# Performance work log

Measured on AMD Instinct MI355X. Metric: run time of the kernel, lower is better.

The kernel has to match this reference:

```python
import jax, jax.numpy as jnp
import numpy as np
import math

N = 5000; K = 30; E = N * K
C_S, C_Z, C_A = 256, 128, 16
H, DH, P, L = 4, 64, 8, 4
NUM_AA = 21
NUM_RBF = 16; D_MIN, D_MAX = 2.0, 22.0
EPS = 1e-8

def _ln(x):
    mu = jnp.mean(x, -1, keepdims=True)
    var = jnp.mean((x - mu) ** 2, -1, keepdims=True)
    return (x - mu) * jax.lax.rsqrt(var + 1e-5)

def _inv_apply(rot, trans, x):
    # rigid invert_apply: R^T (x - t); rot [n,3,3], trans [n,3], x [n,p,3]
    return jnp.einsum('nji,npj->npi', rot, x - trans[:, None, :])

def _rbf(d):
    mu = jnp.linspace(D_MIN, D_MAX, NUM_RBF)
    sigma = (D_MAX - D_MIN) / NUM_RBF
    return jnp.exp(-(((d[..., None] - mu) / sigma) ** 2))

def _dihedral_feats(bb):
    X = bb.reshape(-1, 3)  # [3N,3] N,CA,C chain
    dX = X[1:] - X[:-1]
    U = dX / (jnp.linalg.norm(dX, axis=-1, keepdims=True) + EPS)
    u2, u1, u0 = U[:-2], U[1:-1], U[2:]
    n2 = jnp.cross(u2, u1); n2 = n2 / (jnp.linalg.norm(n2, axis=-1, keepdims=True) + EPS)
    n1 = jnp.cross(u1, u0); n1 = n1 / (jnp.linalg.norm(n1, axis=-1, keepdims=True) + EPS)
    cosD = jnp.clip(jnp.sum(n2 * n1, -1), -1 + 1e-7, 1 - 1e-7)
    D = jnp.sign(jnp.sum(u2 * n1, -1)) * jnp.arccos(cosD)
    D = jnp.pad(D, (1, 2)).reshape(-1, 3)  # [N,3]
    return jnp.concatenate([jnp.cos(D), jnp.sin(D)], -1)  # [N,6]

def _virtual_cb(n, ca, c):
    b = ca - n; cc = c - ca; a = jnp.cross(b, cc)
    return -0.58273431 * a + 0.56802827 * b - 0.54067466 * cc + ca

def _prep(seq, atom14, rot, trans, res_mask, mgm_mask, noising_mask, atom14_exists, edge_index, atom_tab):
    res_f = res_mask.astype(jnp.float32)
    mgm_f = mgm_mask.astype(jnp.float32)
    bb = atom14[:, :3]
    dih = _dihedral_feats(bb)
    seq_oh = jax.nn.one_hot(seq, NUM_AA)
    node_vec = _inv_apply(rot, trans, atom14[:, :4])  # [N,4,3]
    node_raw = jnp.concatenate([dih, mgm_f[:, None], seq_oh * mgm_f[:, None], node_vec.reshape(N, -1)], -1) * res_f[:, None]
    sc = jnp.where(jnp.arange(14) >= 4, mgm_f[:, None], 1.0)  # zero hidden side-chain atoms
    am_f = jnp.where(jnp.arange(14) >= 4, mgm_mask[:, None], atom14_exists).astype(jnp.float32)
    atom_raw = atom_tab[seq] * sc[..., None]  # [N,14,9]
    dsti, srci = edge_index[0], edge_index[1]
    nsrc = noising_mask[srci].astype(jnp.float32); ndst = noising_mask[dsti].astype(jnp.float32)
    cb = _virtual_cb(bb[:, 0], bb[:, 1], bb[:, 2])
    bb4 = jnp.concatenate([bb, cb[:, None]], 1)  # [N,4,3]
    dist = jnp.linalg.norm(bb4[srci][:, :, None] - bb4[dsti][:, None, :] + EPS, axis=-1)  # [E,4,4]
    rbf = _rbf(dist).reshape(E, -1)  # [E,256]
    dpos = (dsti - srci).astype(jnp.float32)
    freq = jnp.exp(jnp.arange(0, 16, 2, dtype=jnp.float32) * (-math.log(10000.0) / 16))
    ang = dpos[:, None] * freq
    pe = jnp.concatenate([jnp.cos(ang), jnp.sin(ang)], -1)  # [E,16]
    bb_local = _inv_apply(rot, trans, bb4)
    src_local = bb_local[srci].reshape(E, -1) * (1 - nsrc)[:, None]
    dst_in_src = jnp.einsum('eji,epj->epi', rot[srci], bb4[dsti] - trans[srci][:, None, :]).reshape(E, -1) * (1 - ndst)[:, None]
    edge_mask = res_mask[srci] & res_mask[dsti]
    edge_raw = jnp.concatenate([ndst[:, None], nsrc[:, None], seq_oh[srci] * (1 - nsrc)[:, None], seq_oh[dsti] * (1 - ndst)[:, None], rbf, pe, src_local, dst_in_src], -1) * edge_mask.astype(jnp.float32)[:, None]
    return node_raw, edge_raw, atom_raw, res_f, am_f, edge_mask

def _mlp3(x, W1, W2, W3):
    return _ln(jax.nn.relu(jax.nn.relu(x @ W1) @ W2) @ W3)

def _net(node_raw, edge_raw, atom_raw, res_f, am_f, edge_mask, rot, trans, edge_index, Wn1, Wn2, Wn3, Wez1, Wez2, Wez3, Wa1, Wa2, Wa3, Wq, Wk, Wv, Wqp, Wkp, Wb, gamma, Wo, Wau, Wt1, Wt2, Wne, We1, We2, Wp1, Wp2, Wmu, Wlv):
    s = _mlp3(node_raw, Wn1, Wn2, Wn3)    # [N,256]
    z = _mlp3(edge_raw, Wez1, Wez2, Wez3) # [E,128]
    af = _mlp3(atom_raw, Wa1, Wa2, Wa3)   # [N,14,16]
    dsti, srci = edge_index[0], edge_index[1]
    em_f = edge_mask.astype(jnp.float32)
    w_pt = math.sqrt(2.0 / (9 * P)); w_l = math.sqrt(1.0 / 3.0)
    for l in range(L):
        q = (s @ Wq[l]).reshape(N, H, DH); k = (s @ Wk[l]).reshape(N, H, DH); v = (s @ Wv[l]).reshape(N, H, DH)
        qp = (s @ Wqp[l]).reshape(N, H, P, 3); kp = (s @ Wkp[l]).reshape(N, H, P, 3)
        qg = jnp.einsum('nij,nhpj->nhpi', rot, qp) + trans[:, None, None, :]
        kg = jnp.einsum('nij,nhpj->nhpi', rot, kp) + trans[:, None, None, :]
        logits = (jnp.sum(q[dsti] * k[srci], -1) * (w_l / math.sqrt(DH))
                  + w_l * (z @ Wb[l])
                  - 0.5 * w_pt * jax.nn.softplus(gamma[l]) * jnp.sum((qg[dsti] - kg[srci]) ** 2, (-2, -1)))
        logits = jnp.where(edge_mask[:, None], logits, -1e9)
        m = jax.ops.segment_max(logits, dsti, num_segments=N)
        a = jnp.exp(logits - m[dsti]) * em_f[:, None]
        a = a / (jax.ops.segment_sum(a, dsti, num_segments=N) + 1e-9)[dsti]
        ov = jax.ops.segment_sum(a[..., None] * v[srci], dsti, num_segments=N).reshape(N, -1)
        og = jax.ops.segment_sum(a[..., None, None] * kg[srci], dsti, num_segments=N)
        ol = jnp.einsum('nji,nhpj->nhpi', rot, og - trans[:, None, None, :])
        on = jnp.sqrt(jnp.sum(ol ** 2, -1) + EPS)
        s = _ln(s + jnp.concatenate([ov, ol.reshape(N, -1), on.reshape(N, -1)], -1) @ Wo[l])
        af = _ln(af + jnp.concatenate([af, jnp.broadcast_to(s[:, None, :], (N, 14, C_S))], -1) @ Wau[l])
        s = _ln(s + jax.nn.relu(s @ Wt1[l]) @ Wt2[l]) * res_f[:, None]
        h = s @ Wne[l]
        z = _ln(jax.nn.relu(jnp.concatenate([z, h[dsti], h[srci]], -1) @ We1[l]) @ We2[l]) * em_f[:, None]
        af = _ln(af + jax.nn.relu(af @ Wp1[l]) @ Wp2[l]) * am_f[..., None]
    return jnp.concatenate([s @ Wmu, s @ Wlv], -1)  # [N,512] = [mu | logvar]

def setup_inputs():
    ks = jax.random.split(jax.random.key(0), 40)
    w = lambda i, shp: jax.random.normal(ks[i], shp, dtype=jnp.float32) * 0.02
    return {
        'seq': jax.random.randint(ks[0], (N,), 0, NUM_AA, dtype=jnp.int32),
        'atom14': jax.random.normal(ks[1], (N, 14, 3), dtype=jnp.float32) * 3.0,
        'rot': jax.random.normal(ks[2], (N, 3, 3), dtype=jnp.float32),
        'trans': jax.random.normal(ks[3], (N, 3), dtype=jnp.float32) * 3.0,
        'res_mask': jnp.ones((N,), dtype=bool),
        'mgm_mask': jax.random.bernoulli(ks[4], 0.5, (N,)),
        'noising_mask': jax.random.bernoulli(ks[5], 0.5, (N,)),
        'atom14_exists': jnp.ones((N, 14), dtype=bool),
        'edge_index': jax.random.randint(ks[6], (2, E), 0, N, dtype=jnp.int32),
        'atom_tab': jax.random.uniform(ks[7], (NUM_AA + 1, 14, 9), dtype=jnp.float32),
        'Wn1': w(8, (40, 512)), 'Wn2': w(9, (512, 512)), 'Wn3': w(10, (512, 256)),
        'Wez1': w(11, (340, 256)), 'Wez2': w(12, (256, 256)), 'Wez3': w(13, (256, 128)),
        'Wa1': w(14, (9, 32)), 'Wa2': w(15, (32, 32)), 'Wa3': w(16, (32, 16)),
        'Wq': w(17, (L, 256, 256)), 'Wk': w(18, (L, 256, 256)), 'Wv': w(19, (L, 256, 256)),
        'Wqp': w(20, (L, 256, H * P * 3)), 'Wkp': w(21, (L, 256, H * P * 3)),
        'Wb': w(22, (L, 128, H)), 'gamma': w(23, (L, H)),
        'Wo': w(24, (L, H * (DH + 4 * P), 256)), 'Wau': w(25, (L, C_A + C_S, C_A)),
        'Wt1': w(26, (L, 256, 256)), 'Wt2': w(27, (L, 256, 256)),
        'Wne': w(28, (L, 256, 128)), 'We1': w(29, (L, 384, 256)), 'We2': w(30, (L, 256, 128)),
        'Wp1': w(31, (L, 16, 16)), 'Wp2': w(32, (L, 16, 16)),
        'Wmu': w(33, (256, 256)), 'Wlv': w(34, (256, 256)),
    }

def reference(seq, atom14, rot, trans, res_mask, mgm_mask, noising_mask, atom14_exists, edge_index, atom_tab, Wn1, Wn2, Wn3, Wez1, Wez2, Wez3, Wa1, Wa2, Wa3, Wq, Wk, Wv, Wqp, Wkp, Wb, gamma, Wo, Wau, Wt1, Wt2, Wne, We1, We2, Wp1, Wp2, Wmu, Wlv):
    prep = _prep(seq, atom14, rot, trans, res_mask, mgm_mask, noising_mask, atom14_exists, edge_index, atom_tab)
    return _net(*prep, rot, trans, edge_index, Wn1, Wn2, Wn3, Wez1, Wez2, Wez3, Wa1, Wa2, Wa3, Wq, Wk, Wv, Wqp, Wkp, Wb, gamma, Wo, Wau, Wt1, Wt2, Wne, We1, We2, Wp1, Wp2, Wmu, Wlv)
```

## Files before the change

kernel.cpp:

```cpp
#include <hip/hip_runtime.h>
#include <hip/hip_bf16.h>

#define NR 5000
#define EE 150000
#define NA14 (NR*14)
#define EPSF 1e-8f

typedef unsigned short ushort;
typedef __attribute__((ext_vector_type(8))) short bf16x8;
typedef __attribute__((ext_vector_type(4))) float f32x4;

#define GLDS16(gp, lp) __builtin_amdgcn_global_load_lds( \
    (__attribute__((address_space(1))) void*)(gp), \
    (__attribute__((address_space(3))) void*)(lp), 16, 0, 0)

static __device__ __forceinline__ float wsum64(float v) {
#pragma unroll
  for (int o = 1; o < 64; o <<= 1) v += __shfl_xor(v, o, 64);
  return v;
}
static __device__ __forceinline__ ushort f2b(float f) {
  union { float f; unsigned u; } x; x.f = f;
  unsigned r = (x.u + 0x7FFF + ((x.u >> 16) & 1)) >> 16;
  return (ushort)r;
// ... 109 lines not shown
    }
    v *= rf;
  }
  nrawb[(size_t)n*64 + c] = f2b(v);
}

__global__ void k_atomraw(const int* __restrict__ seq, const int* __restrict__ mgm,
                          const int* __restrict__ a14ex, const float* __restrict__ atab,
                          float* __restrict__ araw, float* __restrict__ amf) {
  int idx = blockIdx.x * 256 + threadIdx.x;
  if (idx >= NA14) return;
  int n = idx / 14, a = idx - n*14;
  float mg = mgm[n] ? 1.f : 0.f;
  float sc = (a >= 4) ? mg : 1.f;
  const float* src = atab + ((size_t)seq[n]*14 + a) * 9;
#pragma unroll
  for (int j = 0; j < 9; ++j) araw[(size_t)idx*9 + j] = src[j] * sc;
  amf[idx] = (a >= 4) ? mg : (a14ex[idx] ? 1.f : 0.f);
}

__global__ void k_edgeraw(const int* __restrict__ dsti, const int* __restrict__ srci,
                          const int* __restrict__ seq, const int* __restrict__ rmask,
                          const int* __restrict__ nmask, const float* __restrict__ bb4,
                          const float* __restrict__ bbl, const float* __restrict__ rot,
                          const float* __restrict__ trans, ushort* __restrict__ eraw,
                          float* __restrict__ emf, int e0, int cnt) {
  int ei = blockIdx.x * 4 + (threadIdx.x >> 6);
  if (ei >= cnt) return;
  int e = e0 + ei;
  int l = threadIdx.x & 63;
  int d = dsti[e], s = srci[e];
  float em = (rmask[d] && rmask[s]) ? 1.f : 0.f;
  if (l == 0) emf[e] = em;
  float ns = nmask[s] ? 1.f : 0.f;
  float nd = nmask[d] ? 1.f : 0.f;
  ushort* out = eraw + (size_t)ei * 352;

  float dist;
  {
    int p = (l >> 2) & 3, q = l & 3;
    const float* Ps = bb4 + (size_t)s*12 + p*3;
    const float* Pd = bb4 + (size_t)d*12 + q*3;
    float dx = Ps[0]-Pd[0]+EPSF, dy = Ps[1]-Pd[1]+EPSF, dz = Ps[2]-Pd[2]+EPSF;
    dist = sqrtf(dx*dx + dy*dy + dz*dz);
  }
  {
    int q = (l >> 4) & 3;
    float mu = 2.f + (20.f / 15.f) * (float)(l & 15);
#pragma unroll
    for (int p = 0; p < 4; ++p) {
      float dd = __shfl(dist, p*4 + q, 64);
      float tt = (dd - mu) * 0.8f;
      out[44 + p*64 + l] = f2b(expf(-tt * tt) * em);
    }
  }
  if (l < 44) {
    float v;
    if (l == 0) v = nd;
    else if (l == 1) v = ns;
    else if (l < 23) v = (seq[s] == l - 2) ? (1.f - ns) : 0.f;
    else v = (seq[d] == l - 23) ? (1.f - nd) : 0.f;
    out[l] = f2b(v * em);
  }
  if (l < 52) {
    int c = 300 + l;
    float v;
    if (c < 316) {
      int f = c - 300;
      int j = (f < 8) ? f : (f - 8);
      float freq = expf((float)(2*j) * (-9.210340371976184f / 16.f));
      float ang = (float)(d - s) * freq;
      v = (f < 8) ? cosf(ang) : sinf(ang);
    } else if (c < 328) {
      v = bbl[(size_t)s*12 + (c - 316)] * (1.f - ns);
    } else if (c < 340) {
      int u = c - 328; int p = u / 3, i = u - p*3;
      const float* R = rot + (size_t)s*9;
      const float* t = trans + (size_t)s*3;
      const float* Pd = bb4 + (size_t)d*12 + p*3;
      v = (R[0*3+i]*(Pd[0]-t[0]) + R[1*3+i]*(Pd[1]-t[1]) + R[2*3+i]*(Pd[2]-t[2])) * (1.f - nd);
    } else v = 0.f;
    out[c] = f2b(v * em);
  }
}


__global__ void k_zero_int(int* __restrict__ p, int n) {
  int i = blockIdx.x * 256 + threadIdx.x;
  if (i < n) p[i] = 0;
}
__global__ void k_count(const int* __restrict__ dsti, int* __restrict__ cnt) {
  int e = blockIdx.x * 256 + threadIdx.x;
  if (e < EE) atomicAdd(&cnt[dsti[e]], 1);
}
__global__ void k_scan(const int* __restrict__ cnt, int* __restrict__ offs) {
  __shared__ int part[257];
  int t = threadIdx.x;
  const int chunk = (NR + 255) / 256;
  int b = t * chunk;
  int e = min(b + chunk, NR);
  int s = 0;
  for (int i = b; i < e; ++i) s += cnt[i];
  part[t] = s;
  __syncthreads();
  if (t == 0) {
    int r = 0;
    for (int i = 0; i < 256; ++i) { int c = part[i]; part[i] = r; r += c; }
    part[256] = r;
  }
  __syncthreads();
  int r = part[t];
  for (int i = b; i < e; ++i) { offs[i] = r; r += cnt[i]; }
  if (t == 0) offs[NR] = part[256];
}
__global__ void k_place(const int* __restrict__ dsti, const int* __restrict__ offs,
                        int* __restrict__ cnt, int* __restrict__ eord) {
  int e = blockIdx.x * 256 + threadIdx.x;
  if (e < EE) {
    int d = dsti[e];
    int pos = offs[d] + atomicAdd(&cnt[d], 1);
    eord[pos] = e;
  }
}
__global__ void k_sortwave(const int* __restrict__ offs, int* __restrict__ eord) {
  int n = blockIdx.x;
  int l = threadIdx.x;
  int b = offs[n], e = offs[n+1];
  int deg = e - b;
  if (deg <= 1) return;
  if (deg <= 64) {
    int v = (l < deg) ? eord[b + l] : 0x7FFFFFFF;
#pragma unroll
    for (int k = 2; k <= 64; k <<= 1) {
#pragma unroll
      for (int j = k >> 1; j > 0; j >>= 1) {
        int o = __shfl_xor(v, j, 64);
        bool up = ((l & k) == 0);
        bool first = ((l & j) == 0);
        int mn = min(v, o), mx = max(v, o);
        v = (first == up) ? mn : mx;
      }
    }
    if (l < deg) eord[b + l] = v;
  } else if (l == 0) {
    for (int i = b + 1; i < e; ++i) {
      int key = eord[i]; int j = i - 1;
      while (j >= b && eord[j] > key) { eord[j+1] = eord[j]; --j; }
      eord[j+1] = key;
    }
  }
}

__global__ void k_wT(const float* __restrict__ W, ushort* __restrict__ WT,
                     int K, int N, int Kpad, long sstride, long dstride, int L) {
  long idx = (long)blockIdx.x * 256 + threadIdx.x;
  long per = (long)N * Kpad;
  if (idx >= per * L) return;
  int l = (int)(idx / per); long r = idx - (long)l * per;
  int n = (int)(r / Kpad), k = (int)(r - (long)n * Kpad);
  WT[(size_t)l * dstride + (size_t)n * Kpad + k] =
      (k < K) ? f2b(W[(size_t)l * sstride + (size_t)k * N + n]) : (ushort)0;
}

__global__ void k_zero_us(ushort* __restrict__ p, int per, long stride, int L) {
  long idx = (long)blockIdx.x * 256 + threadIdx.x;
  if (idx >= (long)per * L) return;
  int l = (int)(idx / per); int r = (int)(idx - (long)l * per);
  p[(size_t)l * stride + r] = 0;
}

__global__ void k_wbT(const float* __restrict__ Wb, float* __restrict__ WbT) {
  int idx = blockIdx.x * 256 + threadIdx.x;
  if (idx >= 2048) return;
  int l = idx >> 9; int r = idx & 511; int h = r >> 7; int dim = r & 127;
  WbT[idx] = Wb[(size_t)l * 512 + dim * 4 + h];
}
__global__ void k_coef(const float* __restrict__ gam, float* __restrict__ coef) {
  int i = threadIdx.x;
  if (i < 16) coef[i] = 0.5f * (1.f / 6.f) * log1pf(expf(gam[i]));
}

template<int RELU, int OUTBF, int EPADD>
__global__ __launch_bounds__(256) void k_mgemm(
    const ushort* __restrict__ A, const ushort* __restrict__ BT,
    float* __restrict__ Cf, ushort* __restrict__ Cb,
    int M, int Ncols, int Kd, int lda,
    const ushort* __restrict__ HD, const ushort* __restrict__ HS,
    const int* __restrict__ dsti, const int* __restrict__ srci) {
  __shared__ __align__(16) ushort As[2][128][4][8];
  __shared__ __align__(16) ushort Bs[2][128][4][8];
  const int tid = threadIdx.x;
  const int lane = tid & 63;
  const int w = tid >> 6;
  const int wm = (w >> 1) * 64;
  const int wn = (w & 1) * 64;
  const int bm = blockIdx.x * 128;
  const int bn = blockIdx.y * 128;
  const int rl0 = tid >> 2;
  const int sl  = tid & 3;
  const int rl1 = rl0 + 64;
  const int ks0 = (sl - rl0 - (rl0 >> 2)) & 3;
  const int ks1 = (sl - rl1 - (rl1 >> 2)) & 3;
  int ar0 = bm + rl0; if (ar0 >= M) ar0 = M - 1;
  int ar1 = bm + rl1; if (ar1 >= M) ar1 = M - 1;
  const ushort* gA0 = A + (size_t)ar0 * lda + ks0 * 8;
  const ushort* gA1 = A + (size_t)ar1 * lda + ks1 * 8;
  const ushort* gB0 = BT + (size_t)(bn + rl0) * Kd + ks0 * 8;
  const ushort* gB1 = BT + (size_t)(bn + rl1) * Kd + ks1 * 8;

  auto stage = [&](int buf, int k0) {
    GLDS16(gA0 + k0, &As[buf][rl0][sl][0]);
    GLDS16(gB0 + k0, &Bs[buf][rl0][sl][0]);
    GLDS16(gA1 + k0, &As[buf][rl1][sl][0]);
    GLDS16(gB1 + k0, &Bs[buf][rl1][sl][0]);
  };

  f32x4 zero4 = {0.f, 0.f, 0.f, 0.f};
  f32x4 acc[4][4];
#pragma unroll
  for (int i = 0; i < 4; ++i)
#pragma unroll
    for (int j = 0; j < 4; ++j) acc[i][j] = zero4;

  stage(0, 0);
  asm volatile("s_waitcnt vmcnt(0)" ::: "memory");
  __builtin_amdgcn_s_barrier();

  const int nt = Kd >> 5;
  for (int t = 0; t < nt; ++t) {
    int cur = t & 1;
    if (t + 1 < nt) stage(cur ^ 1, (t + 1) << 5);
    {
      const int ksr = lane >> 4, lr = lane & 15;
      bf16x8 af[4], bf[4];
#pragma unroll
      for (int i = 0; i < 4; ++i) {
        int row = wm + i*16 + lr;
        int sa = (ksr + row + (row >> 2)) & 3;
        af[i] = *reinterpret_cast<const bf16x8*>(&As[cur][row][sa][0]);
      }
#pragma unroll
      for (int j = 0; j < 4; ++j) {
        int col = wn + j*16 + lr;
        int sb = (ksr + col + (col >> 2)) & 3;
        bf[j] = *reinterpret_cast<const bf16x8*>(&Bs[cur][col][sb][0]);
      }
#pragma unroll
      for (int i = 0; i < 4; ++i)
#pragma unroll
        for (int j = 0; j < 4; ++j)
          acc[i][j] = __builtin_amdgcn_mfma_f32_16x16x32_bf16(af[i], bf[j], acc[i][j], 0, 0, 0);
    }
    asm volatile("s_waitcnt vmcnt(0) lgkmcnt(0)" ::: "memory");
    __builtin_amdgcn_s_barrier();
  }

  int lr = lane & 15, lg = lane >> 4;
#pragma unroll
  for (int i = 0; i < 4; ++i) {
#pragma unroll
    for (int rg = 0; rg < 4; ++rg) {
      int m = bm + wm + i*16 + lg*4 + rg;
      if (m >= M) continue;
      int de = 0, se = 0;
      if (EPADD) { de = dsti[m]; se = srci[m]; }
#pragma unroll
      for (int j = 0; j < 4; ++j) {
        int cc = bn + wn + j*16 + lr;
        float v = acc[i][j][rg];
        if (EPADD)
          v += b2f(HD[(size_t)de * Ncols + cc]) + b2f(HS[(size_t)se * Ncols + cc]);
        if (RELU) v = fmaxf(v, 0.f);
        if (OUTBF) Cb[(size_t)m * Ncols + cc] = f2b(v);
        else       Cf[(size_t)m * Ncols + cc] = v;
      }
    }
  }
}

__global__ void k_gemm(const float* __restrict__ A, const float* __restrict__ B,
                       float* __restrict__ C, int M, int Ncols, int Kd,
                       int ldc, int coff, int relu) {
  __shared__ float As[16][68];
  __shared__ float Bs[16][64];
  const int tid = threadIdx.x;
  const int bm = blockIdx.x * 64;
  const int bn = blockIdx.y * 64;
  const int tm = tid >> 4;
  const int tn = tid & 15;
  const int arow = tid >> 2;
  const int akq = (tid & 3) << 2;
  const int brow = tid >> 4;
  const int bcol = (tid & 15) << 2;
  float acc[4][4] = {{0.f}};
  const int am = bm + arow;
  for (int k0 = 0; k0 < Kd; k0 += 16) {
    float av[4];
#pragma unroll
    for (int j = 0; j < 4; ++j) {
      int k = k0 + akq + j;
      av[j] = (am < M && k < Kd) ? A[(size_t)am * Kd + k] : 0.f;
    }
#pragma unroll
    for (int j = 0; j < 4; ++j) As[akq + j][arow] = av[j];
    int kb = k0 + brow;
    float bv[4];
    if (kb < Kd) {
#pragma unroll
      for (int j = 0; j < 4; ++j) {
        int c = bn + bcol + j;
        bv[j] = (c < Ncols) ? B[(size_t)kb * Ncols + c] : 0.f;
      }
    } else { bv[0]=bv[1]=bv[2]=bv[3]=0.f; }
    *reinterpret_cast<float4*>(&Bs[brow][bcol]) = make_float4(bv[0],bv[1],bv[2],bv[3]);
    __syncthreads();
#pragma unroll
    for (int kk = 0; kk < 16; ++kk) {
      float4 a4 = *reinterpret_cast<const float4*>(&As[kk][tm << 2]);
      float4 b4 = *reinterpret_cast<const float4*>(&Bs[kk][tn << 2]);
      float aa[4] = {a4.x, a4.y, a4.z, a4.w};
      float bb[4] = {b4.x, b4.y, b4.z, b4.w};
#pragma unroll
      for (int i = 0; i < 4; ++i)
#pragma unroll
        for (int j = 0; j < 4; ++j)
          acc[i][j] = fmaf(aa[i], bb[j], acc[i][j]);
    }
    __syncthreads();
  }
#pragma unroll
  for (int i = 0; i < 4; ++i) {
    int m = bm + (tm << 2) + i;
    if (m >= M) continue;
#pragma unroll
    for (int j = 0; j < 4; ++j) {
      int c = bn + (tn << 2) + j;
      if (c >= Ncols) continue;
      float v = acc[i][j];
      if (relu) v = fmaxf(v, 0.f);
      C[(size_t)m * ldc + coff + c] = v;
    }
  }
}

__global__ void k_small_gemm(const float* __restrict__ A, const float* __restrict__ B,
                             float* __restrict__ C, int M, int Ncols, int Kd, int relu) {
  __shared__ float Ws[1024];
  int t = threadIdx.x;
  int nw = Kd * Ncols;
  for (int i = t; i < nw; i += 256) Ws[i] = B[i];
  __syncthreads();
  int rpb = 256 / Ncols;
  int r = blockIdx.x * rpb + t / Ncols;
  int c = t - (t / Ncols) * Ncols;
  if (r >= M || t >= rpb * Ncols) return;
  const float* a = A + (size_t)r * Kd;
  float s = 0.f;
  for (int k = 0; k < Kd; ++k) s = fmaf(a[k], Ws[k * Ncols + c], s);
  if (relu) s = fmaxf(s, 0.f);
  C[(size_t)r * Ncols + c] = s;
}

__global__ void k_ln(float* __restrict__ dst, ushort* __restrict__ dstb,
                     const float* __restrict__ res, const float* __restrict__ x,
                     const float* __restrict__ rowscale, int M) {
  int r = blockIdx.x * 4 + (threadIdx.x >> 6);
  if (r >= M) return;
  int l = threadIdx.x & 63;
  size_t base = (size_t)r * 256 + l * 4;
  float4 v = *reinterpret_cast<const float4*>(x + base);
  if (res) {
    float4 rv = *reinterpret_cast<const float4*>(res + base);
    v.x += rv.x; v.y += rv.y; v.z += rv.z; v.w += rv.w;
  }
  float s = wsum64(v.x + v.y + v.z + v.w);
  float mu = s * (1.f / 256.f);
  float d0 = v.x-mu, d1 = v.y-mu, d2 = v.z-mu, d3 = v.w-mu;
  float s2 = wsum64(d0*d0 + d1*d1 + d2*d2 + d3*d3);
  float rs = rsqrtf(s2 * (1.f / 256.f) + 1e-5f);
  float sc = rowscale ? rowscale[r] : 1.f;
  float o0 = d0*rs*sc, o1 = d1*rs*sc, o2 = d2*rs*sc, o3 = d3*rs*sc;
  *reinterpret_cast<float4*>(dst + base) = make_float4(o0, o1, o2, o3);
  if (dstb) {
    uint2 p;
    p.x = (unsigned)f2b(o0) | ((unsigned)f2b(o1) << 16);
    p.y = (unsigned)f2b(o2) | ((unsigned)f2b(o3) << 16);
    *reinterpret_cast<uint2*>(dstb + base) = p;
  }
}

__global__ void k_lnz(ushort* __restrict__ z, const float* __restrict__ rowscale) {
  int r = blockIdx.x * 4 + (threadIdx.x >> 6);
  int l = threadIdx.x & 63;
  size_t base = (size_t)r * 128 + l * 2;
  unsigned zw = *reinterpret_cast<const unsigned*>(z + base);
  float v0 = blo(zw), v1 = bhi(zw);
  float s = wsum64(v0 + v1);
  float mu = s * (1.f / 128.f);
  float d0 = v0 - mu, d1 = v1 - mu;
  float s2 = wsum64(d0*d0 + d1*d1);
  float rs = rsqrtf(s2 * (1.f / 128.f) + 1e-5f);
  float sc = rowscale ? rowscale[r] : 1.f;
  unsigned w = (unsigned)f2b(d0*rs*sc) | ((unsigned)f2b(d1*rs*sc) << 16);
  *reinterpret_cast<unsigned*>(z + base) = w;
}

__global__ void k_ln16(float* __restrict__ af, int M) {
  int r = blockIdx.x * 256 + threadIdx.x;
  if (r >= M) return;
  float x[16]; float s = 0.f;
#pragma unroll
  for (int j = 0; j < 16; ++j) { x[j] = af[(size_t)r*16 + j]; s += x[j]; }
  float mu = s * (1.f/16.f);
  float v = 0.f;
#pragma unroll
  for (int j = 0; j < 16; ++j) { float d = x[j]-mu; v += d*d; }
  float rs = rsqrtf(v * (1.f/16.f) + 1e-5f);
#pragma unroll
  for (int j = 0; j < 16; ++j) af[(size_t)r*16 + j] = (x[j]-mu)*rs;
}


__global__ void k_qg(const float* __restrict__ rot, const float* __restrict__ trans,
                     const float* __restrict__ pp,
                     float* __restrict__ qg, float* __restrict__ kg) {
  int idx = blockIdx.x * 256 + threadIdx.x;
  if (idx >= NR * 64) return;
// ... 160 lines not shown
  for (int j = 0; j < 16; ++j) h1[j] = 0.f;
#pragma unroll
  for (int k = 0; k < 16; ++k) {
    float xv = x[k];
#pragma unroll
    for (int j = 0; j < 16; ++j) h1[j] = fmaf(xv, W1[k*16 + j], h1[j]);
  }
#pragma unroll
  for (int j = 0; j < 16; ++j) h1[j] = fmaxf(h1[j], 0.f);
  float h2[16];
#pragma unroll
  for (int j = 0; j < 16; ++j) h2[j] = 0.f;
#pragma unroll
  for (int k = 0; k < 16; ++k) {
    float xv = h1[k];
#pragma unroll
    for (int j = 0; j < 16; ++j) h2[j] = fmaf(xv, W2[k*16 + j], h2[j]);
  }
  float v[16]; float s = 0.f;
#pragma unroll
  for (int j = 0; j < 16; ++j) { v[j] = x[j] + h2[j]; s += v[j]; }
  float mu = s * (1.f/16.f);
  float var = 0.f;
#pragma unroll
  for (int j = 0; j < 16; ++j) { float d = v[j]-mu; var += d*d; }
  float rs = rsqrtf(var * (1.f/16.f) + 1e-5f);
  float am = amf[r];
#pragma unroll
  for (int j = 0; j < 16; ++j) af[(size_t)r*16 + j] = (v[j]-mu)*rs*am;
}

__global__ void k_sentinel(float* __restrict__ out, float val) {
  if (threadIdx.x == 0 && blockIdx.x == 0) out[0] = val;
}


extern "C" void kernel_launch(void* const* d_in, const int* in_sizes, int n_in,
                              void* d_out, int out_size, void* d_ws, size_t ws_size,
                              hipStream_t stream) {
  (void)in_sizes; (void)n_in; (void)out_size;
  const int*   seq    = (const int*)  d_in[0];
  const float* atom14 = (const float*)d_in[1];
  const float* rot    = (const float*)d_in[2];
  const float* trans  = (const float*)d_in[3];
  const int*   rmask  = (const int*)  d_in[4];
  const int*   mgm    = (const int*)  d_in[5];
  const int*   nmask  = (const int*)  d_in[6];
  const int*   a14ex  = (const int*)  d_in[7];
  const int*   eidx   = (const int*)  d_in[8];
  const int*   dsti   = eidx;
  const int*   srci   = eidx + EE;
  const float* atab   = (const float*)d_in[9];
  const float* Wn1 = (const float*)d_in[10];
  const float* Wn2 = (const float*)d_in[11];
  const float* Wn3 = (const float*)d_in[12];
  const float* Wez1 = (const float*)d_in[13];
  const float* Wez2 = (const float*)d_in[14];
  const float* Wez3 = (const float*)d_in[15];
  const float* Wa1 = (const float*)d_in[16];
  const float* Wa2 = (const float*)d_in[17];
  const float* Wa3 = (const float*)d_in[18];
  const float* Wq  = (const float*)d_in[19];
  const float* Wk  = (const float*)d_in[20];
  const float* Wv  = (const float*)d_in[21];
  const float* Wqp = (const float*)d_in[22];
  const float* Wkp = (const float*)d_in[23];
  const float* Wb  = (const float*)d_in[24];
  const float* gam = (const float*)d_in[25];
  const float* Wo  = (const float*)d_in[26];
  const float* Wau = (const float*)d_in[27];
  const float* Wt1 = (const float*)d_in[28];
  const float* Wt2 = (const float*)d_in[29];
  const float* Wne = (const float*)d_in[30];
  const float* We1 = (const float*)d_in[31];
  const float* We2 = (const float*)d_in[32];
  const float* Wp1 = (const float*)d_in[33];
  const float* Wp2 = (const float*)d_in[34];
  const float* Wmu = (const float*)d_in[35];
  const float* Wlv = (const float*)d_in[36];
  float* out = (float*)d_out;

  float* ws = (float*)d_ws;
  size_t WSF = ws_size / sizeof(float);
  size_t off = 0;
  auto alloc = [&](size_t n) { n = (n + 3) & ~(size_t)3; float* p = ws + off; off += n; return p; };

  ushort* Zb  = (ushort*)alloc((size_t)EE * 64);
  float* S    = alloc((size_t)NR * 256);
  ushort* SB  = (ushort*)alloc((size_t)NR * 128);
  float* AF   = alloc((size_t)NA14 * 16);
  float* AMF  = alloc(NA14);
  float* EMF  = alloc(EE);
  float* LOG  = alloc((size_t)EE * 4);
  float* RESF = alloc(NR);
  float* DP   = alloc(3 * NR);
  float* BB4  = alloc((size_t)NR * 12);
  float* BBL  = alloc((size_t)NR * 12);
  ushort* NRAWB = (ushort*)alloc((size_t)NR * 32);
  float* ARAW = alloc((size_t)NA14 * 9);
  ushort* WezT1 = (ushort*)alloc(45056);
  ushort* WezT2 = (ushort*)alloc(32768);
  ushort* WezT3 = (ushort*)alloc(16384);
  ushort* We1zT = (ushort*)alloc(65536);
  ushort* We1dT = (ushort*)alloc(65536);
  ushort* We1sT = (ushort*)alloc(65536);
  ushort* We2T  = (ushort*)alloc(65536);
  ushort* WqkvT = (ushort*)alloc(393216);
  ushort* WppT  = (ushort*)alloc(131072);
  ushort* WoT   = (ushort*)alloc(196608);
  ushort* Wt1T  = (ushort*)alloc(131072);
  ushort* Wt2T  = (ushort*)alloc(131072);
  ushort* WneT  = (ushort*)alloc(65536);
  ushort* WmuLvT= (ushort*)alloc(65536);
  ushort* Wn1T  = (ushort*)alloc(16384);
  ushort* Wn2T  = (ushort*)alloc(131072);
  ushort* Wn3T  = (ushort*)alloc(65536);
  float* WBT  = alloc(2048);
  float* COEF = alloc(16);
  ushort* QKVB= (ushort*)alloc((size_t)NR * 384);
  float* PP   = alloc((size_t)NR * 256);
  float* QG   = alloc((size_t)NR * 96);
  float* KG   = alloc((size_t)NR * 96);
  ushort* CATB= (ushort*)alloc((size_t)NR * 192);
  float* OGb  = alloc((size_t)NR * 96);
  float* NBUF = alloc((size_t)NR * 256);
  ushort* HbB = (ushort*)alloc((size_t)NR * 64);
  ushort* HDb = (ushort*)alloc((size_t)NR * 128);
  ushort* HSb = (ushort*)alloc((size_t)NR * 128);
  float* T1   = alloc((size_t)NR * 16);
  ushort* NB1b = (ushort*)alloc((size_t)NR * 256);
  ushort* NB2b = (ushort*)alloc((size_t)NR * 256);
  ushort* TRHb = (ushort*)alloc((size_t)NR * 128);
  float* AH1  = alloc((size_t)NA14 * 32);
  float* AH2  = alloc((size_t)NA14 * 32);
  int* CNT  = (int*)alloc(NR);
  int* OFFS = (int*)alloc(NR + 1);
  int* EORD = (int*)alloc(EE);
  size_t fixedF = off;

  if (fixedF + (size_t)432 * 1024 > WSF) {
    k_sentinel<<<1, 64, 0, stream>>>(out, 1.0e6f * (float)(ws_size >> 20));
    return;
  }
  float* EAR = ws + fixedF;
  size_t arenaF = WSF - fixedF;
  int CH_P = (int)((arenaF / 432 > (size_t)EE) ? (size_t)EE : arenaF / 432);
  int CH_L = (int)((arenaF / 128 > (size_t)EE) ? (size_t)EE : arenaF / 128);
  ushort* ERb = (ushort*)EAR;
  ushort* B1b = ERb + (size_t)CH_P * 352;
  ushort* B2b = B1b + (size_t)CH_P * 256;
  ushort* EARb = (ushort*)EAR;

  auto wT = [&](const float* W, ushort* WTp, int K, int N, int Kpad,
                long ss, long ds, int L) {
    long tot = (long)N * Kpad * L;
    k_wT<<<(int)((tot + 255) / 256), 256, 0, stream>>>(W, WTp, K, N, Kpad, ss, ds, L);
  };

  wT(Wez1, WezT1, 340, 256, 352, 0, 0, 1);
  wT(Wez2, WezT2, 256, 256, 256, 0, 0, 1);
  wT(Wez3, WezT3, 256, 128, 256, 0, 0, 1);
  wT(Wn1, Wn1T, 40, 512, 64, 0, 0, 1);
  wT(Wn2, Wn2T, 512, 512, 512, 0, 0, 1);
  wT(Wn3, Wn3T, 512, 256, 512, 0, 0, 1);
  wT(We1,         We1zT, 128, 256, 128, 98304, 32768, 4);
  wT(We1 + 32768, We1dT, 128, 256, 128, 98304, 32768, 4);
  wT(We1 + 65536, We1sT, 128, 256, 128, 98304, 32768, 4);
  wT(We2, We2T, 256, 128, 256, 32768, 32768, 4);
  wT(Wo,  WoT,  384, 256, 384, 98304, 98304, 4);
  wT(Wt1, Wt1T, 256, 256, 256, 65536, 65536, 4);
  wT(Wt2, Wt2T, 256, 256, 256, 65536, 65536, 4);
  wT(Wne, WneT, 256, 128, 256, 32768, 32768, 4);
  wT(Wmu, WmuLvT, 256, 256, 256, 0, 0, 1);
  wT(Wlv, WmuLvT + 65536, 256, 256, 256, 0, 0, 1);
  wT(Wq,  WqkvT + 0,       256, 256, 256, 65536, 196608, 4);
  wT(Wk,  WqkvT + 65536,   256, 256, 256, 65536, 196608, 4);
  wT(Wv,  WqkvT + 131072,  256, 256, 256, 65536, 196608, 4);
  wT(Wqp, WppT + 0,        256,  96, 256, 24576, 65536, 4);
  wT(Wkp, WppT + 24576,    256,  96, 256, 24576, 65536, 4);
  k_zero_us<<<(64*256*4 + 255)/256, 256, 0, stream>>>(WppT + 49152, 64*256, 65536, 4);
  k_wbT<<<8, 256, 0, stream>>>(Wb, WBT);
  k_coef<<<1, 64, 0, stream>>>(gam, COEF);

  k_masks<<<(NR + 255) / 256, 256, 0, stream>>>(rmask, RESF);
  k_dihedral<<<(3 * NR + 255) / 256, 256, 0, stream>>>(atom14, DP);
  k_bb4<<<(NR + 255) / 256, 256, 0, stream>>>(atom14, rot, trans, BB4, BBL);
  k_noderaw<<<NR, 64, 0, stream>>>(seq, atom14, rot, trans, DP, rmask, mgm, NRAWB);
  k_atomraw<<<(NA14 + 255) / 256, 256, 0, stream>>>(seq, mgm, a14ex, atab, ARAW, AMF);

  {
    dim3 g1((NR + 127) / 128, 4), g2((NR + 127) / 128, 4), g3((NR + 127) / 128, 2);
    k_mgemm<1,1,0><<<g1, 256, 0, stream>>>(NRAWB, Wn1T, nullptr, NB1b, NR, 512, 64, 64,
                                           nullptr, nullptr, nullptr, nullptr);
    k_mgemm<1,1,0><<<g2, 256, 0, stream>>>(NB1b, Wn2T, nullptr, NB2b, NR, 512, 512, 512,
                                           nullptr, nullptr, nullptr, nullptr);
    k_mgemm<0,0,0><<<g3, 256, 0, stream>>>(NB2b, Wn3T, NBUF, nullptr, NR, 256, 512, 512,
                                           nullptr, nullptr, nullptr, nullptr);
  }
  k_ln<<<(NR + 3) / 4, 256, 0, stream>>>(S, SB, nullptr, NBUF, nullptr, NR);

  k_small_gemm<<<(NA14 + 7) / 8, 256, 0, stream>>>(ARAW, Wa1, AH1, NA14, 32, 9, 1);
  k_small_gemm<<<(NA14 + 7) / 8, 256, 0, stream>>>(AH1, Wa2, AH2, NA14, 32, 32, 1);
  k_small_gemm<<<(NA14 + 15) / 16, 256, 0, stream>>>(AH2, Wa3, AF, NA14, 16, 32, 0);
  k_ln16<<<(NA14 + 255) / 256, 256, 0, stream>>>(AF, NA14);

  k_zero_int<<<(NR + 255) / 256, 256, 0, stream>>>(CNT, NR);
  k_count<<<(EE + 255) / 256, 256, 0, stream>>>(dsti, CNT);
  k_scan<<<1, 256, 0, stream>>>(CNT, OFFS);
  k_zero_int<<<(NR + 255) / 256, 256, 0, stream>>>(CNT, NR);
  k_place<<<(EE + 255) / 256, 256, 0, stream>>>(dsti, OFFS, CNT, EORD);
  k_sortwave<<<NR, 64, 0, stream>>>(OFFS, EORD);

  for (int e0 = 0; e0 < EE; e0 += CH_P) {
    int cnt = (EE - e0 < CH_P) ? (EE - e0) : CH_P;
    k_edgeraw<<<(cnt + 3) / 4, 256, 0, stream>>>(dsti, srci, seq, rmask, nmask,
                                                 BB4, BBL, rot, trans, ERb, EMF, e0, cnt);
    dim3 g1((cnt + 127) / 128, 2), g2((cnt + 127) / 128, 2), g3((cnt + 127) / 128, 1);
    k_mgemm<1,1,0><<<g1, 256, 0, stream>>>(ERb, WezT1, nullptr, B1b, cnt, 256, 352, 352,
                                           nullptr, nullptr, nullptr, nullptr);
    k_mgemm<1,1,0><<<g2, 256, 0, stream>>>(B1b, WezT2, nullptr, B2b, cnt, 256, 256, 256,
                                           nullptr, nullptr, nullptr, nullptr);
    k_mgemm<0,1,0><<<g3, 256, 0, stream>>>(B2b, WezT3, nullptr, Zb + (size_t)e0 * 128,
                                           cnt, 128, 256, 256,
                                           nullptr, nullptr, nullptr, nullptr);
  }
  k_lnz<<<EE / 4, 256, 0, stream>>>(Zb, nullptr);

  for (int l = 0; l < 4; ++l) {
    const ushort* WqkvT_l = WqkvT + (size_t)l * 196608;
    const ushort* WppT_l  = WppT  + (size_t)l * 65536;
    const ushort* WoT_l = WoT + (size_t)l * 98304;
    const float* Wau_l = Wau + (size_t)l * 4352;
    const ushort* Wt1T_l = Wt1T + (size_t)l * 65536;
    const ushort* Wt2T_l = Wt2T + (size_t)l * 65536;
    const ushort* WneT_l = WneT + (size_t)l * 32768;
    const ushort* We1zT_l = We1zT + (size_t)l * 32768;
    const ushort* We1dT_l = We1dT + (size_t)l * 32768;
    const ushort* We1sT_l = We1sT + (size_t)l * 32768;
    const ushort* We2T_l = We2T + (size_t)l * 32768;
    const float* Wp1_l = Wp1 + (size_t)l * 256;
    const float* Wp2_l = Wp2 + (size_t)l * 256;

    {
      dim3 gq((NR + 127) / 128, 6);
      k_mgemm<0,1,0><<<gq, 256, 0, stream>>>(SB, WqkvT_l, nullptr, QKVB, NR, 768, 256, 256,
                                             nullptr, nullptr, nullptr, nullptr);
      dim3 gp((NR + 127) / 128, 2);
      k_mgemm<0,0,0><<<gp, 256, 0, stream>>>(SB, WppT_l, PP, nullptr, NR, 256, 256, 256,
                                             nullptr, nullptr, nullptr, nullptr);
    }
    k_qg<<<(NR * 64 + 255) / 256, 256, 0, stream>>>(rot, trans, PP, QG, KG);
    k_logits<<<EE / 4, 256, 0, stream>>>(dsti, srci, EMF, QKVB, Zb, QG, KG,
                                         WBT + (size_t)l * 512, COEF + (size_t)l * 4, LOG);
    k_attn<<<NR, 64, 0, stream>>>(OFFS, EORD, srci, LOG, EMF, QKVB, KG, CATB, OGb);
    k_olon<<<(NR * 32 + 255) / 256, 256, 0, stream>>>(rot, trans, OGb, CATB);
    {
      dim3 g((NR + 127) / 128, 2);
      k_mgemm<0,0,0><<<g, 256, 0, stream>>>(CATB, WoT_l, NBUF, nullptr, NR, 256, 384, 384,
                                            nullptr, nullptr, nullptr, nullptr);
    }
    k_ln<<<(NR + 3) / 4, 256, 0, stream>>>(S, SB, S, NBUF, nullptr, NR);
    {
      dim3 g((NR + 63) / 64, 1);
      k_gemm<<<g, 256, 0, stream>>>(S, Wau_l + 256, T1, NR, 16, 256, 16, 0, 0);
    }
    k_af_wau<<<(NA14 + 255) / 256, 256, 0, stream>>>(AF, Wau_l, T1);
    {
      dim3 g((NR + 127) / 128, 2);
      k_mgemm<1,1,0><<<g, 256, 0, stream>>>(SB, Wt1T_l, nullptr, TRHb, NR, 256, 256, 256,
                                            nullptr, nullptr, nullptr, nullptr);
      k_mgemm<0,0,0><<<g, 256, 0, stream>>>(TRHb, Wt2T_l, NBUF, nullptr, NR, 256, 256, 256,
                                            nullptr, nullptr, nullptr, nullptr);
    }
    k_ln<<<(NR + 3) / 4, 256, 0, stream>>>(S, SB, S, NBUF, RESF, NR);
    {
      dim3 g((NR + 127) / 128, 1);
      k_mgemm<0,1,0><<<g, 256, 0, stream>>>(SB, WneT_l, nullptr, HbB, NR, 128, 256, 256,
                                            nullptr, nullptr, nullptr, nullptr);
    }
    {
      dim3 g((NR + 127) / 128, 2);
      k_mgemm<0,1,0><<<g, 256, 0, stream>>>(HbB, We1dT_l, nullptr, HDb, NR, 256, 128, 128,
                                            nullptr, nullptr, nullptr, nullptr);
      k_mgemm<0,1,0><<<g, 256, 0, stream>>>(HbB, We1sT_l, nullptr, HSb, NR, 256, 128, 128,
                                            nullptr, nullptr, nullptr, nullptr);
    }
    for (int e0 = 0; e0 < EE; e0 += CH_L) {
      int cnt = (EE - e0 < CH_L) ? (EE - e0) : CH_L;
      dim3 g1((cnt + 127) / 128, 2), g2((cnt + 127) / 128, 1);
      k_mgemm<1,1,1><<<g1, 256, 0, stream>>>(Zb + (size_t)e0 * 128, We1zT_l, nullptr, EARb,
                                             cnt, 256, 128, 128,
                                             HDb, HSb, dsti + e0, srci + e0);
      k_mgemm<0,1,0><<<g2, 256, 0, stream>>>(EARb, We2T_l, nullptr, Zb + (size_t)e0 * 128,
                                             cnt, 128, 256, 256,
                                             nullptr, nullptr, nullptr, nullptr);
    }
    k_lnz<<<EE / 4, 256, 0, stream>>>(Zb, EMF);
    k_af_p<<<(NA14 + 255) / 256, 256, 0, stream>>>(AF, Wp1_l, Wp2_l, AMF);
  }

  {
    dim3 g((NR + 127) / 128, 4);
    k_mgemm<0,0,0><<<g, 256, 0, stream>>>(SB, WmuLvT, out, nullptr, NR, 512, 256, 256,
                                          nullptr, nullptr, nullptr, nullptr);
  }
}
```

Measured before the change: 1.926 ms.

## Permute GEMM output columns for vectorized bf16 stores and matching weight permutation

```diff
diff --git a/kernel.cpp b/kernel.cpp
--- a/kernel.cpp
+++ b/kernel.cpp
@@ -285,14 +285,16 @@
 }
 
 __global__ void k_wT(const float* __restrict__ W, ushort* __restrict__ WT,
-                     int K, int N, int Kpad, long sstride, long dstride, int L) {
+                     int K, int N, int Kpad, long sstride, long dstride, int L,
+                     int perm) {
   long idx = (long)blockIdx.x * 256 + threadIdx.x;
   long per = (long)N * Kpad;
   if (idx >= per * L) return;
   int l = (int)(idx / per); long r = idx - (long)l * per;
   int n = (int)(r / Kpad), k = (int)(r - (long)n * Kpad);
+  int ks = perm ? ((k & ~63) | ((k & 3) * 16 + ((k >> 2) & 15))) : k;
   WT[(size_t)l * dstride + (size_t)n * Kpad + k] =
-      (k < K) ? f2b(W[(size_t)l * sstride + (size_t)k * N + n]) : (ushort)0;
+      (ks < K) ? f2b(W[(size_t)l * sstride + (size_t)ks * N + n]) : (ushort)0;
 }
 
 __global__ void k_zero_us(ushort* __restrict__ p, int per, long stride, int L) {
@@ -313,7 +315,7 @@
   if (i < 16) coef[i] = 0.5f * (1.f / 6.f) * log1pf(expf(gam[i]));
 }
 
-template<int RELU, int OUTBF, int EPADD>
+template<int RELU, int OUTBF, int EPADD, int PERMOUT>
 __global__ __launch_bounds__(256) void k_mgemm(
     const ushort* __restrict__ A, const ushort* __restrict__ BT,
     float* __restrict__ Cf, ushort* __restrict__ Cb,
@@ -389,23 +391,50 @@
   }
 
   int lr = lane & 15, lg = lane >> 4;
-#pragma unroll
-  for (int i = 0; i < 4; ++i) {
-#pragma unroll
-    for (int rg = 0; rg < 4; ++rg) {
-      int m = bm + wm + i*16 + lg*4 + rg;
-      if (m >= M) continue;
-      int de = 0, se = 0;
-      if (EPADD) { de = dsti[m]; se = srci[m]; }
-#pragma unroll
-      for (int j = 0; j < 4; ++j) {
-        int cc = bn + wn + j*16 + lr;
-        float v = acc[i][j][rg];
-        if (EPADD)
-          v += b2f(HD[(size_t)de * Ncols + cc]) + b2f(HS[(size_t)se * Ncols + cc]);
-        if (RELU) v = fmaxf(v, 0.f);
-        if (OUTBF) Cb[(size_t)m * Ncols + cc] = f2b(v);
-        else       Cf[(size_t)m * Ncols + cc] = v;
+  if (PERMOUT) {
+    const int pc = bn + wn + lr * 4;
+#pragma unroll
+    for (int i = 0; i < 4; ++i) {
+#pragma unroll
+      for (int rg = 0; rg < 4; ++rg) {
+        int m = bm + wm + i*16 + lg*4 + rg;
+        if (m >= M) continue;
+        float v0 = acc[i][0][rg], v1 = acc[i][1][rg];
+        float v2 = acc[i][2][rg], v3 = acc[i][3][rg];
+        if (EPADD) {
+          int de = dsti[m], se = srci[m];
+          uint2 hd = *reinterpret_cast<const uint2*>(HD + (size_t)de * Ncols + pc);
+          uint2 hs = *reinterpret_cast<const uint2*>(HS + (size_t)se * Ncols + pc);
+          v0 += blo(hd.x) + blo(hs.x);
+          v1 += bhi(hd.x) + bhi(hs.x);
+          v2 += blo(hd.y) + blo(hs.y);
+          v3 += bhi(hd.y) + bhi(hs.y);
+        }
+        if (RELU) {
+          v0 = fmaxf(v0, 0.f); v1 = fmaxf(v1, 0.f);
+          v2 = fmaxf(v2, 0.f); v3 = fmaxf(v3, 0.f);
+        }
+        uint2 p;
+        p.x = (unsigned)f2b(v0) | ((unsigned)f2b(v1) << 16);
+        p.y = (unsigned)f2b(v2) | ((unsigned)f2b(v3) << 16);
+        *reinterpret_cast<uint2*>(Cb + (size_t)m * Ncols + pc) = p;
+      }
+    }
+  } else {
+#pragma unroll
+    for (int i = 0; i < 4; ++i) {
+#pragma unroll
+      for (int rg = 0; rg < 4; ++rg) {
+        int m = bm + wm + i*16 + lg*4 + rg;
+        if (m >= M) continue;
+#pragma unroll
+        for (int j = 0; j < 4; ++j) {
+          int cc = bn + wn + j*16 + lr;
+          float v = acc[i][j][rg];
+          if (RELU) v = fmaxf(v, 0.f);
+          if (OUTBF) Cb[(size_t)m * Ncols + cc] = f2b(v);
+          else       Cf[(size_t)m * Ncols + cc] = v;
+        }
       }
     }
   }
@@ -872,32 +901,32 @@
   ushort* EARb = (ushort*)EAR;
 
   auto wT = [&](const float* W, ushort* WTp, int K, int N, int Kpad,
-                long ss, long ds, int L) {
+                long ss, long ds, int L, int perm) {
     long tot = (long)N * Kpad * L;
-    k_wT<<<(int)((tot + 255) / 256), 256, 0, stream>>>(W, WTp, K, N, Kpad, ss, ds, L);
+    k_wT<<<(int)((tot + 255) / 256), 256, 0, stream>>>(W, WTp, K, N, Kpad, ss, ds, L, perm);
   };
 
-  wT(Wez1, WezT1, 340, 256, 352, 0, 0, 1);
-  wT(Wez2, WezT2, 256, 256, 256, 0, 0, 1);
-  wT(Wez3, WezT3, 256, 128, 256, 0, 0, 1);
-  wT(Wn1, Wn1T, 40, 512, 64, 0, 0, 1);
-  wT(Wn2, Wn2T, 512, 512, 512, 0, 0, 1);
-  wT(Wn3, Wn3T, 512, 256, 512, 0, 0, 1);
-  wT(We1,         We1zT, 128, 256, 128, 98304, 32768, 4);
-  wT(We1 + 32768, We1dT, 128, 256, 128, 98304, 32768, 4);
-  wT(We1 + 65536, We1sT, 128, 256, 128, 98304, 32768, 4);
-  wT(We2, We2T, 256, 128, 256, 32768, 32768, 4);
-  wT(Wo,  WoT,  384, 256, 384, 98304, 98304, 4);
-  wT(Wt1, Wt1T, 256, 256, 256, 65536, 65536, 4);
-  wT(Wt2, Wt2T, 256, 256, 256, 65536, 65536, 4);
-  wT(Wne, WneT, 256, 128, 256, 32768, 32768, 4);
-  wT(Wmu, WmuLvT, 256, 256, 256, 0, 0, 1);
-  wT(Wlv, WmuLvT + 65536, 256, 256, 256, 0, 0, 1);
-  wT(Wq,  WqkvT + 0,       256, 256, 256, 65536, 196608, 4);
-  wT(Wk,  WqkvT + 65536,   256, 256, 256, 65536, 196608, 4);
-  wT(Wv,  WqkvT + 131072,  256, 256, 256, 65536, 196608, 4);
-  wT(Wqp, WppT + 0,        256,  96, 256, 24576, 65536, 4);
-  wT(Wkp, WppT + 24576,    256,  96, 256, 24576, 65536, 4);
+  wT(Wez1, WezT1, 340, 256, 352, 0, 0, 1, 0);
+  wT(Wez2, WezT2, 256, 256, 256, 0, 0, 1, 1);
+  wT(Wez3, WezT3, 256, 128, 256, 0, 0, 1, 1);
+  wT(Wn1, Wn1T, 40, 512, 64, 0, 0, 1, 0);
+  wT(Wn2, Wn2T, 512, 512, 512, 0, 0, 1, 1);
+  wT(Wn3, Wn3T, 512, 256, 512, 0, 0, 1, 1);
+  wT(We1,         We1zT, 128, 256, 128, 98304, 32768, 4, 0);
+  wT(We1 + 32768, We1dT, 128, 256, 128, 98304, 32768, 4, 0);
+  wT(We1 + 65536, We1sT, 128, 256, 128, 98304, 32768, 4, 0);
+  wT(We2, We2T, 256, 128, 256, 32768, 32768, 4, 1);
+  wT(Wo,  WoT,  384, 256, 384, 98304, 98304, 4, 0);
+  wT(Wt1, Wt1T, 256, 256, 256, 65536, 65536, 4, 0);
+  wT(Wt2, Wt2T, 256, 256, 256, 65536, 65536, 4, 1);
+  wT(Wne, WneT, 256, 128, 256, 32768, 32768, 4, 0);
+  wT(Wmu, WmuLvT, 256, 256, 256, 0, 0, 1, 0);
+  wT(Wlv, WmuLvT + 65536, 256, 256, 256, 0, 0, 1, 0);
+  wT(Wq,  WqkvT + 0,       256, 256, 256, 65536, 196608, 4, 0);
+  wT(Wk,  WqkvT + 65536,   256, 256, 256, 65536, 196608, 4, 0);
+  wT(Wv,  WqkvT + 131072,  256, 256, 256, 65536, 196608, 4, 0);
+  wT(Wqp, WppT + 0,        256,  96, 256, 24576, 65536, 4, 0);
+  wT(Wkp, WppT + 24576,    256,  96, 256, 24576, 65536, 4, 0);
   k_zero_us<<<(64*256*4 + 255)/256, 256, 0, stream>>>(WppT + 49152, 64*256, 65536, 4);
   k_wbT<<<8, 256, 0, stream>>>(Wb, WBT);
   k_coef<<<1, 64, 0, stream>>>(gam, COEF);
@@ -910,12 +939,12 @@
 
   {
     dim3 g1((NR + 127) / 128, 4), g2((NR + 127) / 128, 4), g3((NR + 127) / 128, 2);
-    k_mgemm<1,1,0><<<g1, 256, 0, stream>>>(NRAWB, Wn1T, nullptr, NB1b, NR, 512, 64, 64,
-                                           nullptr, nullptr, nullptr, nullptr);
-    k_mgemm<1,1,0><<<g2, 256, 0, stream>>>(NB1b, Wn2T, nullptr, NB2b, NR, 512, 512, 512,
-                                           nullptr, nullptr, nullptr, nullptr);
-    k_mgemm<0,0,0><<<g3, 256, 0, stream>>>(NB2b, Wn3T, NBUF, nullptr, NR, 256, 512, 512,
-                                           nullptr, nullptr, nullptr, nullptr);
+    k_mgemm<1,1,0,1><<<g1, 256, 0, stream>>>(NRAWB, Wn1T, nullptr, NB1b, NR, 512, 64, 64,
+                                             nullptr, nullptr, nullptr, nullptr);
+    k_mgemm<1,1,0,1><<<g2, 256, 0, stream>>>(NB1b, Wn2T, nullptr, NB2b, NR, 512, 512, 512,
+                                             nullptr, nullptr, nullptr, nullptr);
+    k_mgemm<0,0,0,0><<<g3, 256, 0, stream>>>(NB2b, Wn3T, NBUF, nullptr, NR, 256, 512, 512,
+                                             nullptr, nullptr, nullptr, nullptr);
   }
   k_ln<<<(NR + 3) / 4, 256, 0, stream>>>(S, SB, nullptr, NBUF, nullptr, NR);
 
@@ -936,13 +965,13 @@
     k_edgeraw<<<(cnt + 3) / 4, 256, 0, stream>>>(dsti, srci, seq, rmask, nmask,
                                                  BB4, BBL, rot, trans, ERb, EMF, e0, cnt);
     dim3 g1((cnt + 127) / 128, 2), g2((cnt + 127) / 128, 2), g3((cnt + 127) / 128, 1);
-    k_mgemm<1,1,0><<<g1, 256, 0, stream>>>(ERb, WezT1, nullptr, B1b, cnt, 256, 352, 352,
-                                           nullptr, nullptr, nullptr, nullptr);
-    k_mgemm<1,1,0><<<g2, 256, 0, stream>>>(B1b, WezT2, nullptr, B2b, cnt, 256, 256, 256,
-                                           nullptr, nullptr, nullptr, nullptr);
-    k_mgemm<0,1,0><<<g3, 256, 0, stream>>>(B2b, WezT3, nullptr, Zb + (size_t)e0 * 128,
-                                           cnt, 128, 256, 256,
-                                           nullptr, nullptr, nullptr, nullptr);
+    k_mgemm<1,1,0,1><<<g1, 256, 0, stream>>>(ERb, WezT1, nullptr, B1b, cnt, 256, 352, 352,
+                                             nullptr, nullptr, nullptr, nullptr);
+    k_mgemm<1,1,0,1><<<g2, 256, 0, stream>>>(B1b, WezT2, nullptr, B2b, cnt, 256, 256, 256,
+                                             nullptr, nullptr, nullptr, nullptr);
+    k_mgemm<0,1,0,0><<<g3, 256, 0, stream>>>(B2b, WezT3, nullptr, Zb + (size_t)e0 * 128,
+                                             cnt, 128, 256, 256,
+                                             nullptr, nullptr, nullptr, nullptr);
   }
   k_lnz<<<EE / 4, 256, 0, stream>>>(Zb, nullptr);
 
@@ -963,11 +992,11 @@
 
     {
       dim3 gq((NR + 127) / 128, 6);
-      k_mgemm<0,1,0><<<gq, 256, 0, stream>>>(SB, WqkvT_l, nullptr, QKVB, NR, 768, 256, 256,
-                                             nullptr, nullptr, nullptr, nullptr);
+      k_mgemm<0,1,0,0><<<gq, 256, 0, stream>>>(SB, WqkvT_l, nullptr, QKVB, NR, 768, 256, 256,
+                                               nullptr, nullptr, nullptr, nullptr);
       dim3 gp((NR + 127) / 128, 2);
-      k_mgemm<0,0,0><<<gp, 256, 0, stream>>>(SB, WppT_l, PP, nullptr, NR, 256, 256, 256,
-                                             nullptr, nullptr, nullptr, nullptr);
+      k_mgemm<0,0,0,0><<<gp, 256, 0, stream>>>(SB, WppT_l, PP, nullptr, NR, 256, 256, 256,
+                                               nullptr, nullptr, nullptr, nullptr);
     }
     k_qg<<<(NR * 64 + 255) / 256, 256, 0, stream>>>(rot, trans, PP, QG, KG);
     k_logits<<<EE / 4, 256, 0, stream>>>(dsti, srci, EMF, QKVB, Zb, QG, KG,
@@ -976,8 +1005,8 @@
     k_olon<<<(NR * 32 + 255) / 256, 256, 0, stream>>>(rot, trans, OGb, CATB);
     {
       dim3 g((NR + 127) / 128, 2);
-      k_mgemm<0,0,0><<<g, 256, 0, stream>>>(CATB, WoT_l, NBUF, nullptr, NR, 256, 384, 384,
-                                            nullptr, nullptr, nullptr, nullptr);
+      k_mgemm<0,0,0,0><<<g, 256, 0, stream>>>(CATB, WoT_l, NBUF, nullptr, NR, 256, 384, 384,
+                                              nullptr, nullptr, nullptr, nullptr);
     }
     k_ln<<<(NR + 3) / 4, 256, 0, stream>>>(S, SB, S, NBUF, nullptr, NR);
     {
@@ -987,33 +1016,33 @@
     k_af_wau<<<(NA14 + 255) / 256, 256, 0, stream>>>(AF, Wau_l, T1);
     {
       dim3 g((NR + 127) / 128, 2);
-      k_mgemm<1,1,0><<<g, 256, 0, stream>>>(SB, Wt1T_l, nullptr, TRHb, NR, 256, 256, 256,
-                                            nullptr, nullptr, nullptr, nullptr);
-      k_mgemm<0,0,0><<<g, 256, 0, stream>>>(TRHb, Wt2T_l, NBUF, nullptr, NR, 256, 256, 256,
-                                            nullptr, nullptr, nullptr, nullptr);
+      k_mgemm<1,1,0,1><<<g, 256, 0, stream>>>(SB, Wt1T_l, nullptr, TRHb, NR, 256, 256, 256,
+                                              nullptr, nullptr, nullptr, nullptr);
+      k_mgemm<0,0,0,0><<<g, 256, 0, stream>>>(TRHb, Wt2T_l, NBUF, nullptr, NR, 256, 256, 256,
+                                              nullptr, nullptr, nullptr, nullptr);
     }
     k_ln<<<(NR + 3) / 4, 256, 0, stream>>>(S, SB, S, NBUF, RESF, NR);
     {
       dim3 g((NR + 127) / 128, 1);
-      k_mgemm<0,1,0><<<g, 256, 0, stream>>>(SB, WneT_l, nullptr, HbB, NR, 128, 256, 256,
-                                            nullptr, nullptr, nullptr, nullptr);
+      k_mgemm<0,1,0,0><<<g, 256, 0, stream>>>(SB, WneT_l, nullptr, HbB, NR, 128, 256, 256,
+                                              nullptr, nullptr, nullptr, nullptr);
     }
     {
       dim3 g((NR + 127) / 128, 2);
-      k_mgemm<0,1,0><<<g, 256, 0, stream>>>(HbB, We1dT_l, nullptr, HDb, NR, 256, 128, 128,
-                                            nullptr, nullptr, nullptr, nullptr);
-      k_mgemm<0,1,0><<<g, 256, 0, stream>>>(HbB, We1sT_l, nullptr, HSb, NR, 256, 128, 128,
-                                            nullptr, nullptr, nullptr, nullptr);
+      k_mgemm<0,1,0,1><<<g, 256, 0, stream>>>(HbB, We1dT_l, nullptr, HDb, NR, 256, 128, 128,
+                                              nullptr, nullptr, nullptr, nullptr);
+      k_mgemm<0,1,0,1><<<g, 256, 0, stream>>>(HbB, We1sT_l, nullptr, HSb, NR, 256, 128, 128,
+                                              nullptr, nullptr, nullptr, nullptr);
     }
     for (int e0 = 0; e0 < EE; e0 += CH_L) {
       int cnt = (EE - e0 < CH_L) ? (EE - e0) : CH_L;
       dim3 g1((cnt + 127) / 128, 2), g2((cnt + 127) / 128, 1);
-      k_mgemm<1,1,1><<<g1, 256, 0, stream>>>(Zb + (size_t)e0 * 128, We1zT_l, nullptr, EARb,
-                                             cnt, 256, 128, 128,
-                                             HDb, HSb, dsti + e0, srci + e0);
-      k_mgemm<0,1,0><<<g2, 256, 0, stream>>>(EARb, We2T_l, nullptr, Zb + (size_t)e0 * 128,
-                                             cnt, 128, 256, 256,
-                                             nullptr, nullptr, nullptr, nullptr);
+      k_mgemm<1,1,1,1><<<g1, 256, 0, stream>>>(Zb + (size_t)e0 * 128, We1zT_l, nullptr, EARb,
+                                               cnt, 256, 128, 128,
+                                               HDb, HSb, dsti + e0, srci + e0);
+      k_mgemm<0,1,0,0><<<g2, 256, 0, stream>>>(EARb, We2T_l, nullptr, Zb + (size_t)e0 * 128,
+                                               cnt, 128, 256, 256,
+                                               nullptr, nullptr, nullptr, nullptr);
     }
     k_lnz<<<EE / 4, 256, 0, stream>>>(Zb, EMF);
     k_af_p<<<(NA14 + 255) / 256, 256, 0, stream>>>(AF, Wp1_l, Wp2_l, AMF);
@@ -1021,7 +1050,7 @@
 
   {
     dim3 g((NR + 127) / 128, 4);
-    k_mgemm<0,0,0><<<g, 256, 0, stream>>>(SB, WmuLvT, out, nullptr, NR, 512, 256, 256,
-                                          nullptr, nullptr, nullptr, nullptr);
-  }
-}
+    k_mgemm<0,0,0,0><<<g, 256, 0, stream>>>(SB, WmuLvT, out, nullptr, NR, 512, 256, 256,
+                                            nullptr, nullptr, nullptr, nullptr);
+  }
+}
```

Result: no change. 1.922 ms (-0.2%).
